# Optimization experiments

Measured on AMD Instinct MI355X. Metric: run time of the kernel, lower is better.

The kernel has to match this reference:

```python
import jax, jax.numpy as jnp
import numpy as np

EMBED = 768
HEADS = 12
HEAD_DIM = EMBED // HEADS
NUM_BUCKETS = 32
MAX_DISTANCE = 128


def _relative_buckets(tgt_len, src_len):
    ctx = jnp.arange(tgt_len)[:, None]
    mem = jnp.arange(src_len)[None, :]
    rel = mem - ctx                                  # [T, S]
    nb = NUM_BUCKETS // 2                            # 16
    buckets = (rel > 0).astype(jnp.int32) * nb
    rp = jnp.abs(rel)
    max_exact = nb // 2                              # 8
    is_small = rp < max_exact
    rp_safe = jnp.maximum(rp, 1).astype(jnp.float32)
    large = max_exact + (
        jnp.log(rp_safe / max_exact) / np.log(MAX_DISTANCE / max_exact) * (nb - max_exact)
    ).astype(jnp.int32)
    large = jnp.minimum(large, nb - 1)
    buckets = buckets + jnp.where(is_small, rp, large)
    return buckets                                   # [T, S] int32


def setup_inputs() -> dict:
    key = jax.random.key(0)
    ks = jax.random.split(key, 12)
    T, B, E = 2048, 2, EMBED
    def xavier(k, shape, gain=1.0):
        fan_in, fan_out = shape[0], shape[1]
        a = gain * np.sqrt(6.0 / (fan_in + fan_out))
        return jax.random.uniform(k, shape, jnp.float32, -a, a)
    g = 1.0 / np.sqrt(2.0)
    return {
        "query": jax.random.normal(ks[0], (T, B, E), jnp.float32),
        "key": jax.random.normal(ks[1], (T, B, E), jnp.float32),
        "value": jax.random.normal(ks[2], (T, B, E), jnp.float32),
        "key_padding_mask": jnp.zeros((B, T), dtype=bool),
        # weights stored [in, out] (transpose of torch Linear)
        "Wq": xavier(ks[3], (E, E), g), "bq": jnp.zeros((E,), jnp.float32),
        "Wk": xavier(ks[4], (E, E), g), "bk": jnp.zeros((E,), jnp.float32),
        "Wv": xavier(ks[5], (E, E), g), "bv": jnp.zeros((E,), jnp.float32),
        "Wo": xavier(ks[6], (E, E), 1.0), "bo": jnp.zeros((E,), jnp.float32),
        "rel_bias": jax.random.normal(ks[7], (NUM_BUCKETS, HEADS), jnp.float32)
        * np.sqrt(2.0 / (NUM_BUCKETS + HEADS)),
    }


def reference(query, key, value, key_padding_mask, Wq, bq, Wk, bk, Wv, bv, Wo, bo, rel_bias):
    T, B, E = query.shape
    S = key.shape[0]
    scaling = HEAD_DIM ** -0.5
    q = (query @ Wq + bq) * scaling
    k = key @ Wk + bk
    v = value @ Wv + bv
    # [T,B,E] -> [B,H,T,D]
    def split_heads(x, L):
        return x.reshape(L, B, HEADS, HEAD_DIM).transpose(1, 2, 0, 3)
    qh, kh, vh = split_heads(q, T), split_heads(k, S), split_heads(v, S)
    # T5 relative position bias: [H, T, S]
    buckets = _relative_buckets(T, S)
    position_bias = rel_bias[buckets].transpose(2, 0, 1)  # [H,T,S]
    scores = jnp.einsum("bhtd,bhsd->bhts", qh, kh) + position_bias[None]
    scores = jnp.where(key_padding_mask[:, None, None, :], -jnp.inf, scores)
    probs = jax.nn.softmax(scores, axis=-1)
    attn = jnp.einsum("bhts,bhsd->bhtd", probs, vh)
    attn = attn.transpose(2, 0, 1, 3).reshape(T, B, E)
    return attn @ Wo + bo
```

## Files before the change

kernel.cpp:

```cpp
#include <hip/hip_runtime.h>
#include <hip/hip_bf16.h>

typedef __bf16 bf16;
typedef __bf16 bf16x8 __attribute__((ext_vector_type(8)));
typedef float f32x4 __attribute__((ext_vector_type(4)));

#define EMB 768
#define NH 12
#define HD 64
#define SEQ 2048
#define NBATCH 2
#define NREL (2 * SEQ - 1)

__device__ __forceinline__ int swz(int bo) { return bo ^ ((bo >> 3) & 0x70); }
__device__ __forceinline__ int swz256(int bo) { return bo ^ ((bo >> 4) & 0x70); }
__device__ __forceinline__ int kpos(int s) {
  return (s & 0x23) | ((s & 0x04) << 2) | ((s & 0x18) >> 1);
}

typedef __attribute__((address_space(3))) unsigned int lds_u32;
typedef __attribute__((address_space(1))) unsigned int glb_u32;
__device__ __forceinline__ void gld16(const void* g, void* l) {
  __builtin_amdgcn_global_load_lds((const glb_u32*)g, (lds_u32*)l, 16, 0, 0);
}

__global__ void k_bias_table(const float* __restrict__ rel_bias,
                             float* __restrict__ bias_tab) {
  int i = blockIdx.x * 256 + threadIdx.x;
  if (i >= NREL) return;
  int rel = i - (SEQ - 1);
  int bkt = (rel > 0) ? 16 : 0;
  int rp = rel < 0 ? -rel : rel;
  if (rp < 8) {
    bkt += rp;
  } else {
    float lf = (logf((float)rp * 0.125f) / 2.7725887222397811f) * 8.0f;
    int large = 8 + (int)lf;
    bkt += (large < 15) ? large : 15;
  }
  for (int h = 0; h < NH; ++h)
    bias_tab[h * NREL + i] = rel_bias[bkt * NH + h];
}

__global__ void k_maskbits(const unsigned char* __restrict__ mask,
                           unsigned long long* __restrict__ mbits) {
  int wid = blockIdx.x * 4 + (threadIdx.x >> 6);
  int lane = threadIdx.x & 63;
  int b = wid >> 5, wd = wid & 31;
  unsigned long long m = __ballot(mask[b * SEQ + wd * 64 + lane] != 0);
  if (lane == 0) mbits[wid] = m;
}

__global__ __launch_bounds__(256) void k_cvt_x(
    const float* __restrict__ Xq, const float* __restrict__ Xk,
    const float* __restrict__ Xv, bf16* __restrict__ ximg) {
  const int z = blockIdx.z;
  const float* X = z == 0 ? Xq : z == 1 ? Xk : Xv;
  const int m0 = blockIdx.x * 128, k0 = blockIdx.y * 64;
  char* img = (char*)ximg + ((size_t)(z * 32 + blockIdx.x) * 12 + blockIdx.y) * 16384;
#pragma unroll
  for (int it = 0; it < 4; ++it) {
    int i = threadIdx.x + it * 256;
    int mr = i >> 3, kc8 = (i & 7) * 8;
    const float* xp = X + (size_t)(m0 + mr) * EMB + k0 + kc8;
    float4 f0 = *(const float4*)xp, f1 = *(const float4*)(xp + 4);
    bf16x8 hh;
    hh[0] = (bf16)f0.x; hh[1] = (bf16)f0.y; hh[2] = (bf16)f0.z; hh[3] = (bf16)f0.w;
    hh[4] = (bf16)f1.x; hh[5] = (bf16)f1.y; hh[6] = (bf16)f1.z; hh[7] = (bf16)f1.w;
    *(bf16x8*)(img + swz(mr * 128 + kc8 * 2)) = hh;
  }
}

__global__ __launch_bounds__(256) void k_cvt_w(
    const float* __restrict__ Wq, const float* __restrict__ Wk,
    const float* __restrict__ Wv, const float* __restrict__ Wo,
    bf16* __restrict__ wimg) {
  __shared__ __align__(16) bf16 T[64 * 128];
  const int z = blockIdx.z;
  const float* W = z == 0 ? Wq : z == 1 ? Wk : z == 2 ? Wv : Wo;
  const int nb = blockIdx.x, ks = blockIdx.y;
  const int n0 = nb * 128, k0 = ks * 64;
  const int tid = threadIdx.x;
  {
    int kk = tid >> 2, nn0 = (tid & 3) * 32;
    const float* wp = W + (size_t)(k0 + kk) * EMB + n0 + nn0;
#pragma unroll
    for (int jq = 0; jq < 4; ++jq) {
      float4 f0 = *(const float4*)(wp + jq * 8);
      float4 f1 = *(const float4*)(wp + jq * 8 + 4);
      bf16x8 hh;
      hh[0] = (bf16)f0.x; hh[1] = (bf16)f0.y; hh[2] = (bf16)f0.z; hh[3] = (bf16)f0.w;
      hh[4] = (bf16)f1.x; hh[5] = (bf16)f1.y; hh[6] = (bf16)f1.z; hh[7] = (bf16)f1.w;
      *(bf16x8*)((char*)T + swz256(kk * 256 + (nn0 + jq * 8) * 2)) = hh;
    }
  }
  __syncthreads();
  {
    int nr = tid >> 1, kh = tid & 1;
    char* img = (char*)wimg + ((size_t)(z * 6 + nb) * 12 + ks) * 16384;
#pragma unroll
    for (int jq = 0; jq < 4; ++jq) {
      union { bf16 e[8]; uint4 u; } pk;
#pragma unroll
      for (int q = 0; q < 8; ++q)
        pk.e[q] = *(const bf16*)((char*)T + swz256((kh * 32 + jq * 8 + q) * 256 + nr * 2));
      *(uint4*)(img + swz(nr * 128 + (kh * 32 + jq * 8) * 2)) = pk.u;
    }
  }
}

__global__ __launch_bounds__(256) void k_proj_qkv(
    const bf16* __restrict__ ximg, const bf16* __restrict__ wimg,
    const float* __restrict__ bq, const float* __restrict__ bk,
    const float* __restrict__ bv, bf16* __restrict__ oq,
    bf16* __restrict__ gk, bf16* __restrict__ gv) {
  __shared__ __align__(16) bf16 AB[2][2][8192];
  const int z = blockIdx.z;
  const float* bias = z == 0 ? bq : z == 1 ? bk : bv;
  const float scale = z == 0 ? 0.125f : 1.0f;
  const int mb = blockIdx.x, nb = blockIdx.y;
  const int m0 = mb * 128, n0 = nb * 128;
  const int tid = threadIdx.x, lane = tid & 63, w = tid >> 6;
  const int c = lane & 15, g = lane >> 4;
  const int mo = (w >> 1) * 64, no = (w & 1) * 64;
  const char* abase = (const char*)ximg + (size_t)(z * 32 + mb) * 12 * 16384;
  const char* bbase = (const char*)wimg + (size_t)(z * 6 + nb) * 12 * 16384;

#define PISSUE(KS, BUF) do {                                               \
    const char* a_ = abase + (size_t)(KS) * 16384;                         \
    const char* b_ = bbase + (size_t)(KS) * 16384;                         \
    _Pragma("unroll") for (int ch = 0; ch < 4; ++ch) {                     \
      int ck = w * 4 + ch;                                                 \
      gld16(a_ + ck * 1024 + lane * 16, (char*)AB[BUF][0] + ck * 1024);    \
      gld16(b_ + ck * 1024 + lane * 16, (char*)AB[BUF][1] + ck * 1024);    \
    }                                                                      \
  } while (0)

  PISSUE(0, 0);
  f32x4 acc[4][4] = {};
  asm volatile("s_waitcnt vmcnt(0)" ::: "memory");
  __syncthreads();
  for (int ks = 0; ks < 12; ++ks) {
    const int cur = ks & 1;
    if (ks < 11) PISSUE(ks + 1, cur ^ 1);
    const char* As = (const char*)AB[cur][0];
    const char* Bs = (const char*)AB[cur][1];
    __builtin_amdgcn_s_setprio(1);
#pragma unroll
    for (int kk = 0; kk < 2; ++kk) {
      bf16x8 av[4], bvf[4];
#pragma unroll
      for (int mf = 0; mf < 4; ++mf)
        av[mf] = *(const bf16x8*)(As + swz((mo + mf * 16 + c) * 128 + kk * 64 + g * 16));
#pragma unroll
      for (int nf = 0; nf < 4; ++nf)
        bvf[nf] = *(const bf16x8*)(Bs + swz((no + nf * 16 + c) * 128 + kk * 64 + g * 16));
#pragma unroll
      for (int mf = 0; mf < 4; ++mf)
#pragma unroll
        for (int nf = 0; nf < 4; ++nf)
          acc[mf][nf] = __builtin_amdgcn_mfma_f32_16x16x32_bf16(bvf[nf], av[mf], acc[mf][nf], 0, 0, 0);
    }
    __builtin_amdgcn_s_setprio(0);
    if (ks < 11) {
      asm volatile("s_waitcnt vmcnt(0)" ::: "memory");
      __syncthreads();
    }
  }
#pragma unroll
  for (int nf = 0; nf < 4; ++nf) {
    int n = n0 + no + nf * 16 + g * 4;
    float4 b4 = *(const float4*)&bias[n];
#pragma unroll
    for (int mf = 0; mf < 4; ++mf) {
      int m = m0 + mo + mf * 16 + c;
      float v0 = (acc[mf][nf][0] + b4.x) * scale;
      float v1 = (acc[mf][nf][1] + b4.y) * scale;
      float v2 = (acc[mf][nf][2] + b4.z) * scale;
      float v3 = (acc[mf][nf][3] + b4.w) * scale;
      if (z == 0) {
        union { bf16 e[4]; uint2 u; } pk;
        pk.e[0] = (bf16)v0; pk.e[1] = (bf16)v1; pk.e[2] = (bf16)v2; pk.e[3] = (bf16)v3;
        *(uint2*)(oq + (size_t)m * EMB + n) = pk.u;
      } else if (z == 1) {
        int t = m >> 1, bb = m & 1;
        int hh = n >> 6, d = n & 63;
        union { bf16 e[4]; uint2 u; } pk;
        pk.e[0] = (bf16)v0; pk.e[1] = (bf16)v1; pk.e[2] = (bf16)v2; pk.e[3] = (bf16)v3;
        char* base = (char*)gk + ((size_t)(bb * NH + hh) * 32 + (t >> 6)) * 8192;
        *(uint2*)(base + swz(kpos(t & 63) * 128 + (d & ~7) * 2) + (d & 4) * 2) = pk.u;
      } else {
        int s = m >> 1, bb = m & 1;
        int hh = n >> 6, d0 = n & 63;
        char* base = (char*)gv + ((size_t)(bb * NH + hh) * 32 + (s >> 6)) * 8192;
        int sc2 = (s & 63) * 2;
        *(bf16*)(base + (((d0 + 0) * 128 + sc2) ^ (((d0 + 0) & 7) << 4))) = (bf16)v0;
        *(bf16*)(base + (((d0 + 1) * 128 + sc2) ^ (((d0 + 1) & 7) << 4))) = (bf16)v1;
        *(bf16*)(base + (((d0 + 2) * 128 + sc2) ^ (((d0 + 2) & 7) << 4))) = (bf16)v2;
        *(bf16*)(base + (((d0 + 3) * 128 + sc2) ^ (((d0 + 3) & 7) << 4))) = (bf16)v3;
      }
    }
  }
#undef PISSUE
}

__global__ __launch_bounds__(256) void k_proj_out(
    const bf16* __restrict__ aimg, const bf16* __restrict__ wimg,
    const float* __restrict__ bias, float* __restrict__ out) {
  __shared__ __align__(16) bf16 AB[2][2][8192];
  const int mb = blockIdx.x, nb = blockIdx.y;
  const int m0 = mb * 128, n0 = nb * 128;
  const int tid = threadIdx.x, lane = tid & 63, w = tid >> 6;
  const int c = lane & 15, g = lane >> 4;
  const int mo = (w >> 1) * 64, no = (w & 1) * 64;
  const char* abase = (const char*)aimg + (size_t)mb * 12 * 16384;
  const char* bbase = (const char*)wimg + (size_t)(3 * 6 + nb) * 12 * 16384;

#define PISSUE(KS, BUF) do {                                               \
    const char* a_ = abase + (size_t)(KS) * 16384;                         \
    const char* b_ = bbase + (size_t)(KS) * 16384;                         \
    _Pragma("unroll") for (int ch = 0; ch < 4; ++ch) {                     \
      int ck = w * 4 + ch;                                                 \
      gld16(a_ + ck * 1024 + lane * 16, (char*)AB[BUF][0] + ck * 1024);    \
      gld16(b_ + ck * 1024 + lane * 16, (char*)AB[BUF][1] + ck * 1024);    \
    }                                                                      \
  } while (0)

  PISSUE(0, 0);
  f32x4 acc[4][4] = {};
  asm volatile("s_waitcnt vmcnt(0)" ::: "memory");
  __syncthreads();
  for (int ks = 0; ks < 12; ++ks) {
    const int cur = ks & 1;
    if (ks < 11) PISSUE(ks + 1, cur ^ 1);
    const char* As = (const char*)AB[cur][0];
    const char* Bs = (const char*)AB[cur][1];
    __builtin_amdgcn_s_setprio(1);
#pragma unroll
    for (int kk = 0; kk < 2; ++kk) {
      bf16x8 av[4], bvf[4];
#pragma unroll
      for (int mf = 0; mf < 4; ++mf)
        av[mf] = *(const bf16x8*)(As + swz((mo + mf * 16 + c) * 128 + kk * 64 + g * 16));
#pragma unroll
      for (int nf = 0; nf < 4; ++nf)
        bvf[nf] = *(const bf16x8*)(Bs + swz((no + nf * 16 + c) * 128 + kk * 64 + g * 16));
#pragma unroll
      for (int mf = 0; mf < 4; ++mf)
#pragma unroll
        for (int nf = 0; nf < 4; ++nf)
          acc[mf][nf] = __builtin_amdgcn_mfma_f32_16x16x32_bf16(bvf[nf], av[mf], acc[mf][nf], 0, 0, 0);
    }
    __builtin_amdgcn_s_setprio(0);
    if (ks < 11) {
      asm volatile("s_waitcnt vmcnt(0)" ::: "memory");
      __syncthreads();
    }
  }
#pragma unroll
  for (int nf = 0; nf < 4; ++nf) {
    int n = n0 + no + nf * 16 + g * 4;
    float4 b4 = *(const float4*)&bias[n];
#pragma unroll
    for (int mf = 0; mf < 4; ++mf) {
      int m = m0 + mo + mf * 16 + c;
      float4 v;
      v.x = acc[mf][nf][0] + b4.x;
      v.y = acc[mf][nf][1] + b4.y;
      v.z = acc[mf][nf][2] + b4.z;
      v.w = acc[mf][nf][3] + b4.w;
      *(float4*)(out + (size_t)m * EMB + n) = v;
    }
  }
#undef PISSUE
}

__global__ __launch_bounds__(256, 4) void k_attn(
    const bf16* __restrict__ qb, const bf16* __restrict__ gk,
    const bf16* __restrict__ gv, const unsigned long long* __restrict__ mbits,
    const float* __restrict__ bias_tab, bf16* __restrict__ aimg) {
  __shared__ __align__(16) bf16 KV[2][2][4096];
  __shared__ float Bslow[384];
  const int bh = blockIdx.x;
  const int b = bh / NH, h = bh % NH;
  const int t0 = blockIdx.y * 64;
  const int tid = threadIdx.x;
  const int lane = tid & 63, w = tid >> 6;
  const int c = lane & 15, g = lane >> 4;
  const float NEGINF = -__builtin_inff();
  const int tl = w * 16 + c;

  const char* kimg = (const char*)gk + (size_t)bh * 32 * 8192;
  const char* vimg = (const char*)gv + (size_t)bh * 32 * 8192;

#define ISSUE(IT, BUF) do {                                                  \
    const char* ks_ = kimg + (size_t)(IT) * 8192;                            \
    const char* vs_ = vimg + (size_t)(IT) * 8192;                            \
    _Pragma("unroll") for (int jj = 0; jj < 2; ++jj) {                       \
      int ch = w * 2 + jj;                                                   \
      gld16(ks_ + ch * 1024 + lane * 16, (char*)KV[BUF][0] + ch * 1024);     \
      gld16(vs_ + ch * 1024 + lane * 16, (char*)KV[BUF][1] + ch * 1024);     \
    }                                                                        \
  } while (0)

  ISSUE(0, 0);
  bf16x8 qf[2];
  {
    const bf16* qp = qb + (size_t)((t0 + tl) * NBATCH + b) * EMB + h * 64 + g * 8;
    qf[0] = *(const bf16x8*)qp;
    qf[1] = *(const bf16x8*)(qp + 32);
  }
  const float* btab = bias_tab + h * NREL + (SEQ - 1);
  for (int j = tid; j < 384; j += 256) Bslow[j] = btab[j - 192];
  const float cpos = btab[SEQ - 1];
  const float cneg = btab[-(SEQ - 1)];

  float m_p = -1e30f, l_p = 0.f;
  f32x4 o[4] = {};

  asm volatile("s_waitcnt vmcnt(0)" ::: "memory");
  __syncthreads();

  for (int it = 0; it < SEQ / 64; ++it) {
    const int cur = it & 1;
    if (it < SEQ / 64 - 1) ISSUE(it + 1, cur ^ 1);
    const unsigned long long mb = mbits[b * 32 + it];
    const char* Ks = (const char*)KV[cur][0];
    const char* Vs = (const char*)KV[cur][1];

    f32x4 sacc[4] = {};
    __builtin_amdgcn_s_setprio(1);
#pragma unroll
    for (int kk = 0; kk < 2; ++kk) {
#pragma unroll
      for (int nf = 0; nf < 4; ++nf) {
        bf16x8 kf = *(const bf16x8*)(Ks + swz((nf * 16 + c) * 128 + kk * 64 + g * 16));
        sacc[nf] = __builtin_amdgcn_mfma_f32_16x16x32_bf16(kf, qf[kk], sacc[nf], 0, 0, 0);
      }
    }
    __builtin_amdgcn_s_setprio(0);

    const int s0 = it * 64;
    const int d = s0 - t0;
    const bool slow = (d > -192) && (d < 192);
    const float cb = slow ? 0.f : (d >= 192 ? cpos : cneg);

    float rmax = NEGINF;
    if (slow) {
      const int bidx = d - tl + 192;
#pragma unroll
      for (int nf = 0; nf < 4; ++nf) {
        int sb = 32 * (nf >> 1) + g * 8 + (nf & 1) * 4;
#pragma unroll
        for (int r = 0; r < 4; ++r) sacc[nf][r] += Bslow[bidx + sb + r];
      }
    }
    if (mb) {
#pragma unroll
      for (int nf = 0; nf < 4; ++nf) {
        int sb = 32 * (nf >> 1) + g * 8 + (nf & 1) * 4;
#pragma unroll
        for (int r = 0; r < 4; ++r)
          if ((mb >> (sb + r)) & 1) sacc[nf][r] = NEGINF;
      }
    }
#pragma unroll
    for (int nf = 0; nf < 4; ++nf)
#pragma unroll
      for (int r = 0; r < 4; ++r) rmax = fmaxf(rmax, sacc[nf][r]);
    rmax = fmaxf(rmax, __shfl_xor(rmax, 16, 64));
    rmax = fmaxf(rmax, __shfl_xor(rmax, 32, 64));
    const float rm = rmax + cb;

    if (!__all(rm <= m_p + 8.0f)) {
      float m_new = fmaxf(m_p, rm);
      float scl = __expf(m_p - m_new);
      m_p = m_new;
      l_p *= scl;
#pragma unroll
      for (int r = 0; r < 4; ++r) {
        float so = __shfl(scl, g * 4 + r, 64);
#pragma unroll
        for (int nf2 = 0; nf2 < 4; ++nf2) o[nf2][r] *= so;
      }
    }
    const float msh = m_p - cb;
    float rsum = 0.f;
    bf16x8 pa[2];
#pragma unroll
    for (int kk = 0; kk < 2; ++kk)
#pragma unroll
      for (int j = 0; j < 8; ++j) {
        float e = __expf(sacc[2 * kk + (j >> 2)][j & 3] - msh);
        rsum += e;
        pa[kk][j] = (bf16)e;
      }
    rsum += __shfl_xor(rsum, 16, 64);
    rsum += __shfl_xor(rsum, 32, 64);
    l_p += rsum;

    __builtin_amdgcn_s_setprio(1);
#pragma unroll
    for (int kk = 0; kk < 2; ++kk) {
#pragma unroll
      for (int nf2 = 0; nf2 < 4; ++nf2) {
        bf16x8 vbf = *(const bf16x8*)(Vs + swz((nf2 * 16 + c) * 128 + kk * 64 + g * 16));
        o[nf2] = __builtin_amdgcn_mfma_f32_16x16x32_bf16(pa[kk], vbf, o[nf2], 0, 0, 0);
      }
    }
    __builtin_amdgcn_s_setprio(0);

    if (it < SEQ / 64 - 1) {
      asm volatile("s_waitcnt vmcnt(0)" ::: "memory");
      __syncthreads();
    }
  }
#pragma unroll
  for (int r = 0; r < 4; ++r) {
    float lo = __shfl(l_p, g * 4 + r, 64);
    float inv = 1.0f / lo;
    int t = t0 + w * 16 + g * 4 + r;
    int m = t * NBATCH + b;
    char* base = (char*)aimg + ((size_t)(m >> 7) * 12 + h) * 16384;
    int mr128 = (m & 127) * 128;
#pragma unroll
    for (int nf2 = 0; nf2 < 4; ++nf2) {
      int dd = nf2 * 16 + c;
      *(bf16*)(base + swz(mr128 + dd * 2)) = (bf16)(o[nf2][r] * inv);
    }
  }
#undef ISSUE
}

extern "C" void kernel_launch(void* const* d_in, const int* in_sizes, int n_in,
                              void* d_out, int out_size, void* d_ws, size_t ws_size,
                              hipStream_t stream) {
  const float* query = (const float*)d_in[0];
  const float* key_ = (const float*)d_in[1];
  const float* value = (const float*)d_in[2];
  const unsigned char* kpm = (const unsigned char*)d_in[3];
  const float* Wq = (const float*)d_in[4];
  const float* bq = (const float*)d_in[5];
  const float* Wk = (const float*)d_in[6];
  const float* bk = (const float*)d_in[7];
  const float* Wv = (const float*)d_in[8];
  const float* bv = (const float*)d_in[9];
  const float* Wo = (const float*)d_in[10];
  const float* bo = (const float*)d_in[11];
  const float* rel_bias = (const float*)d_in[12];
  float* out = (float*)d_out;

  char* ws = (char*)d_ws;
  const size_t SZb = (size_t)SEQ * NBATCH * EMB * sizeof(bf16);
  const size_t WIMG = (size_t)4 * 6 * 12 * 16384;
  bf16* qbb = (bf16*)(ws);
  bf16* gkb = (bf16*)(ws + SZb);
  bf16* gvb = (bf16*)(ws + 2 * SZb);
  bf16* wimg = (bf16*)(ws + 3 * SZb);
  float* bias_tab = (float*)(ws + 3 * SZb + WIMG);
  unsigned long long* mbits =
      (unsigned long long*)(ws + 3 * SZb + WIMG + 196608);
  bf16* ximg = (bf16*)(ws + 3 * SZb + WIMG + 196608 + 512);
  bf16* aimg = ximg;

  k_bias_table<<<16, 256, 0, stream>>>(rel_bias, bias_tab);
  k_maskbits<<<16, 256, 0, stream>>>(kpm, mbits);
  k_cvt_w<<<dim3(6, 12, 4), 256, 0, stream>>>(Wq, Wk, Wv, Wo, wimg);
  k_cvt_x<<<dim3(32, 12, 3), 256, 0, stream>>>(query, key_, value, ximg);
  k_proj_qkv<<<dim3(32, 6, 3), 256, 0, stream>>>(
      ximg, wimg, bq, bk, bv, qbb, gkb, gvb);
  k_attn<<<dim3(NBATCH * NH, SEQ / 64), 256, 0, stream>>>(
      qbb, gkb, gvb, mbits, bias_tab, aimg);
  k_proj_out<<<dim3(32, 6), 256, 0, stream>>>(aimg, wimg, bo, out);
}
```

Baseline: 110.2 us.

## Merge setup kernels, use exp2 softmax, compute row sums via MFMA

Merges the four preprocessing kernels (bias table, mask bits, X and W conversion) into one launch that branches on block index. Folds log2(e) into the Q scale and the bias table so the softmax can call exp2f directly. Computes row sums of P with an MFMA against a ones vector instead of scalar adds plus cross-lane shuffles, and loosens the rescale threshold to match base-2 units. This saves launch overhead and some VALU and shuffle work, at the cost of two extra MFMAs per tile and row sums taken from the bf16-rounded probabilities.

```diff
diff --git a/kernel.cpp b/kernel.cpp
--- a/kernel.cpp
+++ b/kernel.cpp
@@ -11,6 +11,7 @@
 #define SEQ 2048
 #define NBATCH 2
 #define NREL (2 * SEQ - 1)
+#define LOG2E 1.44269504088896f
 
 __device__ __forceinline__ int swz(int bo) { return bo ^ ((bo >> 3) & 0x70); }
 __device__ __forceinline__ int swz256(int bo) { return bo ^ ((bo >> 4) & 0x70); }
@@ -24,88 +25,88 @@
   __builtin_amdgcn_global_load_lds((const glb_u32*)g, (lds_u32*)l, 16, 0, 0);
 }
 
-__global__ void k_bias_table(const float* __restrict__ rel_bias,
-                             float* __restrict__ bias_tab) {
-  int i = blockIdx.x * 256 + threadIdx.x;
-  if (i >= NREL) return;
-  int rel = i - (SEQ - 1);
-  int bkt = (rel > 0) ? 16 : 0;
-  int rp = rel < 0 ? -rel : rel;
-  if (rp < 8) {
-    bkt += rp;
-  } else {
-    float lf = (logf((float)rp * 0.125f) / 2.7725887222397811f) * 8.0f;
-    int large = 8 + (int)lf;
-    bkt += (large < 15) ? large : 15;
-  }
-  for (int h = 0; h < NH; ++h)
-    bias_tab[h * NREL + i] = rel_bias[bkt * NH + h];
-}
-
-__global__ void k_maskbits(const unsigned char* __restrict__ mask,
-                           unsigned long long* __restrict__ mbits) {
-  int wid = blockIdx.x * 4 + (threadIdx.x >> 6);
-  int lane = threadIdx.x & 63;
-  int b = wid >> 5, wd = wid & 31;
-  unsigned long long m = __ballot(mask[b * SEQ + wd * 64 + lane] != 0);
-  if (lane == 0) mbits[wid] = m;
-}
-
-__global__ __launch_bounds__(256) void k_cvt_x(
+__global__ __launch_bounds__(256) void k_setup(
     const float* __restrict__ Xq, const float* __restrict__ Xk,
-    const float* __restrict__ Xv, bf16* __restrict__ ximg) {
-  const int z = blockIdx.z;
-  const float* X = z == 0 ? Xq : z == 1 ? Xk : Xv;
-  const int m0 = blockIdx.x * 128, k0 = blockIdx.y * 64;
-  char* img = (char*)ximg + ((size_t)(z * 32 + blockIdx.x) * 12 + blockIdx.y) * 16384;
-#pragma unroll
-  for (int it = 0; it < 4; ++it) {
-    int i = threadIdx.x + it * 256;
-    int mr = i >> 3, kc8 = (i & 7) * 8;
-    const float* xp = X + (size_t)(m0 + mr) * EMB + k0 + kc8;
-    float4 f0 = *(const float4*)xp, f1 = *(const float4*)(xp + 4);
-    bf16x8 hh;
-    hh[0] = (bf16)f0.x; hh[1] = (bf16)f0.y; hh[2] = (bf16)f0.z; hh[3] = (bf16)f0.w;
-    hh[4] = (bf16)f1.x; hh[5] = (bf16)f1.y; hh[6] = (bf16)f1.z; hh[7] = (bf16)f1.w;
-    *(bf16x8*)(img + swz(mr * 128 + kc8 * 2)) = hh;
-  }
-}
-
-__global__ __launch_bounds__(256) void k_cvt_w(
-    const float* __restrict__ Wq, const float* __restrict__ Wk,
-    const float* __restrict__ Wv, const float* __restrict__ Wo,
-    bf16* __restrict__ wimg) {
+    const float* __restrict__ Xv, const float* __restrict__ Wq,
+    const float* __restrict__ Wk, const float* __restrict__ Wv,
+    const float* __restrict__ Wo, const unsigned char* __restrict__ mask,
+    const float* __restrict__ rel_bias, bf16* __restrict__ ximg,
+    bf16* __restrict__ wimg, float* __restrict__ bias_tab,
+    unsigned long long* __restrict__ mbits) {
   __shared__ __align__(16) bf16 T[64 * 128];
-  const int z = blockIdx.z;
-  const float* W = z == 0 ? Wq : z == 1 ? Wk : z == 2 ? Wv : Wo;
-  const int nb = blockIdx.x, ks = blockIdx.y;
-  const int n0 = nb * 128, k0 = ks * 64;
+  const int idx = blockIdx.x;
   const int tid = threadIdx.x;
-  {
-    int kk = tid >> 2, nn0 = (tid & 3) * 32;
-    const float* wp = W + (size_t)(k0 + kk) * EMB + n0 + nn0;
-#pragma unroll
-    for (int jq = 0; jq < 4; ++jq) {
-      float4 f0 = *(const float4*)(wp + jq * 8);
-      float4 f1 = *(const float4*)(wp + jq * 8 + 4);
+  if (idx < 1152) {
+    const int z = idx / 384, rem = idx % 384;
+    const int mb = rem % 32, ks = rem / 32;
+    const float* X = z == 0 ? Xq : z == 1 ? Xk : Xv;
+    const int m0 = mb * 128, k0 = ks * 64;
+    char* img = (char*)ximg + ((size_t)(z * 32 + mb) * 12 + ks) * 16384;
+#pragma unroll
+    for (int it = 0; it < 4; ++it) {
+      int i = tid + it * 256;
+      int mr = i >> 3, kc8 = (i & 7) * 8;
+      const float* xp = X + (size_t)(m0 + mr) * EMB + k0 + kc8;
+      float4 f0 = *(const float4*)xp, f1 = *(const float4*)(xp + 4);
       bf16x8 hh;
       hh[0] = (bf16)f0.x; hh[1] = (bf16)f0.y; hh[2] = (bf16)f0.z; hh[3] = (bf16)f0.w;
       hh[4] = (bf16)f1.x; hh[5] = (bf16)f1.y; hh[6] = (bf16)f1.z; hh[7] = (bf16)f1.w;
-      *(bf16x8*)((char*)T + swz256(kk * 256 + (nn0 + jq * 8) * 2)) = hh;
-    }
-  }
-  __syncthreads();
-  {
-    int nr = tid >> 1, kh = tid & 1;
-    char* img = (char*)wimg + ((size_t)(z * 6 + nb) * 12 + ks) * 16384;
-#pragma unroll
-    for (int jq = 0; jq < 4; ++jq) {
-      union { bf16 e[8]; uint4 u; } pk;
-#pragma unroll
-      for (int q = 0; q < 8; ++q)
-        pk.e[q] = *(const bf16*)((char*)T + swz256((kh * 32 + jq * 8 + q) * 256 + nr * 2));
-      *(uint4*)(img + swz(nr * 128 + (kh * 32 + jq * 8) * 2)) = pk.u;
-    }
+      *(bf16x8*)(img + swz(mr * 128 + kc8 * 2)) = hh;
+    }
+  } else if (idx < 1440) {
+    const int i = idx - 1152;
+    const int z = i / 72, rem = i % 72;
+    const int nb = rem % 6, ks = rem / 6;
+    const float* W = z == 0 ? Wq : z == 1 ? Wk : z == 2 ? Wv : Wo;
+    const int n0 = nb * 128, k0 = ks * 64;
+    {
+      int kk = tid >> 2, nn0 = (tid & 3) * 32;
+      const float* wp = W + (size_t)(k0 + kk) * EMB + n0 + nn0;
+#pragma unroll
+      for (int jq = 0; jq < 4; ++jq) {
+        float4 f0 = *(const float4*)(wp + jq * 8);
+        float4 f1 = *(const float4*)(wp + jq * 8 + 4);
+        bf16x8 hh;
+        hh[0] = (bf16)f0.x; hh[1] = (bf16)f0.y; hh[2] = (bf16)f0.z; hh[3] = (bf16)f0.w;
+        hh[4] = (bf16)f1.x; hh[5] = (bf16)f1.y; hh[6] = (bf16)f1.z; hh[7] = (bf16)f1.w;
+        *(bf16x8*)((char*)T + swz256(kk * 256 + (nn0 + jq * 8) * 2)) = hh;
+      }
+    }
+    __syncthreads();
+    {
+      int nr = tid >> 1, kh = tid & 1;
+      char* img = (char*)wimg + ((size_t)(z * 6 + nb) * 12 + ks) * 16384;
+#pragma unroll
+      for (int jq = 0; jq < 4; ++jq) {
+        union { bf16 e[8]; uint4 u; } pk;
+#pragma unroll
+        for (int q = 0; q < 8; ++q)
+          pk.e[q] = *(const bf16*)((char*)T + swz256((kh * 32 + jq * 8 + q) * 256 + nr * 2));
+        *(uint4*)(img + swz(nr * 128 + (kh * 32 + jq * 8) * 2)) = pk.u;
+      }
+    }
+  } else if (idx < 1456) {
+    int i = (idx - 1440) * 256 + tid;
+    if (i < NREL) {
+      int rel = i - (SEQ - 1);
+      int bkt = (rel > 0) ? 16 : 0;
+      int rp = rel < 0 ? -rel : rel;
+      if (rp < 8) {
+        bkt += rp;
+      } else {
+        float lf = (logf((float)rp * 0.125f) / 2.7725887222397811f) * 8.0f;
+        int large = 8 + (int)lf;
+        bkt += (large < 15) ? large : 15;
+      }
+      for (int h = 0; h < NH; ++h)
+        bias_tab[h * NREL + i] = rel_bias[bkt * NH + h] * LOG2E;
+    }
+  } else {
+    int wid = (idx - 1456) * 4 + (tid >> 6);
+    int lane = tid & 63;
+    int b = wid >> 5, wd = wid & 31;
+    unsigned long long m = __ballot(mask[b * SEQ + wd * 64 + lane] != 0);
+    if (lane == 0) mbits[wid] = m;
   }
 }
 
@@ -117,7 +118,7 @@
   __shared__ __align__(16) bf16 AB[2][2][8192];
   const int z = blockIdx.z;
   const float* bias = z == 0 ? bq : z == 1 ? bk : bv;
-  const float scale = z == 0 ? 0.125f : 1.0f;
+  const float scale = z == 0 ? 0.125f * LOG2E : 1.0f;
   const int mb = blockIdx.x, nb = blockIdx.y;
   const int m0 = mb * 128, n0 = nb * 128;
   const int tid = threadIdx.x, lane = tid & 63, w = tid >> 6;
@@ -315,15 +316,20 @@
   const float cpos = btab[SEQ - 1];
   const float cneg = btab[-(SEQ - 1)];
 
-  float m_p = -1e30f, l_p = 0.f;
+  bf16x8 ones8;
+#pragma unroll
+  for (int j = 0; j < 8; ++j) ones8[j] = (bf16)1.0f;
+
+  float m_p = -1e30f;
+  f32x4 lacc = {0.f, 0.f, 0.f, 0.f};
   f32x4 o[4] = {};
 
   asm volatile("s_waitcnt vmcnt(0)" ::: "memory");
   __syncthreads();
 
-  for (int it = 0; it < SEQ / 64; ++it) {
+  for (int it = 0; it < 32; ++it) {
     const int cur = it & 1;
-    if (it < SEQ / 64 - 1) ISSUE(it + 1, cur ^ 1);
+    if (it < 31) ISSUE(it + 1, cur ^ 1);
     const unsigned long long mb = mbits[b * 32 + it];
     const char* Ks = (const char*)KV[cur][0];
     const char* Vs = (const char*)KV[cur][1];
@@ -345,7 +351,6 @@
     const bool slow = (d > -192) && (d < 192);
     const float cb = slow ? 0.f : (d >= 192 ? cpos : cneg);
 
-    float rmax = NEGINF;
     if (slow) {
       const int bidx = d - tl + 192;
 #pragma unroll
@@ -364,42 +369,38 @@
           if ((mb >> (sb + r)) & 1) sacc[nf][r] = NEGINF;
       }
     }
-#pragma unroll
-    for (int nf = 0; nf < 4; ++nf)
-#pragma unroll
-      for (int r = 0; r < 4; ++r) rmax = fmaxf(rmax, sacc[nf][r]);
+    f32x4 mx;
+#pragma unroll
+    for (int r = 0; r < 4; ++r)
+      mx[r] = fmaxf(fmaxf(sacc[0][r], sacc[1][r]), fmaxf(sacc[2][r], sacc[3][r]));
+    float rmax = fmaxf(fmaxf(mx[0], mx[1]), fmaxf(mx[2], mx[3]));
     rmax = fmaxf(rmax, __shfl_xor(rmax, 16, 64));
     rmax = fmaxf(rmax, __shfl_xor(rmax, 32, 64));
     const float rm = rmax + cb;
 
-    if (!__all(rm <= m_p + 8.0f)) {
+    if (!__all(rm <= m_p + 11.5f)) {
       float m_new = fmaxf(m_p, rm);
-      float scl = __expf(m_p - m_new);
+      float scl = exp2f(m_p - m_new);
       m_p = m_new;
-      l_p *= scl;
 #pragma unroll
       for (int r = 0; r < 4; ++r) {
         float so = __shfl(scl, g * 4 + r, 64);
+        lacc[r] *= so;
 #pragma unroll
         for (int nf2 = 0; nf2 < 4; ++nf2) o[nf2][r] *= so;
       }
     }
     const float msh = m_p - cb;
-    float rsum = 0.f;
     bf16x8 pa[2];
 #pragma unroll
     for (int kk = 0; kk < 2; ++kk)
 #pragma unroll
-      for (int j = 0; j < 8; ++j) {
-        float e = __expf(sacc[2 * kk + (j >> 2)][j & 3] - msh);
-        rsum += e;
-        pa[kk][j] = (bf16)e;
-      }
-    rsum += __shfl_xor(rsum, 16, 64);
-    rsum += __shfl_xor(rsum, 32, 64);
-    l_p += rsum;
+      for (int j = 0; j < 8; ++j)
+        pa[kk][j] = (bf16)exp2f(sacc[2 * kk + (j >> 2)][j & 3] - msh);
 
     __builtin_amdgcn_s_setprio(1);
+    lacc = __builtin_amdgcn_mfma_f32_16x16x32_bf16(pa[0], ones8, lacc, 0, 0, 0);
+    lacc = __builtin_amdgcn_mfma_f32_16x16x32_bf16(pa[1], ones8, lacc, 0, 0, 0);
 #pragma unroll
     for (int kk = 0; kk < 2; ++kk) {
 #pragma unroll
@@ -410,15 +411,14 @@
     }
     __builtin_amdgcn_s_setprio(0);
 
-    if (it < SEQ / 64 - 1) {
+    if (it < 31) {
       asm volatile("s_waitcnt vmcnt(0)" ::: "memory");
       __syncthreads();
     }
   }
 #pragma unroll
   for (int r = 0; r < 4; ++r) {
-    float lo = __shfl(l_p, g * 4 + r, 64);
-    float inv = 1.0f / lo;
+    float inv = 1.0f / lacc[r];
     int t = t0 + w * 16 + g * 4 + r;
     int m = t * NBATCH + b;
     char* base = (char*)aimg + ((size_t)(m >> 7) * 12 + h) * 16384;
@@ -463,10 +463,8 @@
   bf16* ximg = (bf16*)(ws + 3 * SZb + WIMG + 196608 + 512);
   bf16* aimg = ximg;
 
-  k_bias_table<<<16, 256, 0, stream>>>(rel_bias, bias_tab);
-  k_maskbits<<<16, 256, 0, stream>>>(kpm, mbits);
-  k_cvt_w<<<dim3(6, 12, 4), 256, 0, stream>>>(Wq, Wk, Wv, Wo, wimg);
-  k_cvt_x<<<dim3(32, 12, 3), 256, 0, stream>>>(query, key_, value, ximg);
+  k_setup<<<1472, 256, 0, stream>>>(query, key_, value, Wq, Wk, Wv, Wo,
+                                    kpm, rel_bias, ximg, wimg, bias_tab, mbits);
   k_proj_qkv<<<dim3(32, 6, 3), 256, 0, stream>>>(
       ximg, wimg, bq, bk, bv, qbb, gkb, gvb);
   k_attn<<<dim3(NBATCH * NH, SEQ / 64), 256, 0, stream>>>(
```

Measured after the change: 108.3 us. About the same (-1.7%).
